# Kernel optimization log

Hardware: AMD Instinct MI355X
Metric: run time of the kernel (lower is better)

The kernel has to match this reference:

```python
import jax, jax.numpy as jnp
import numpy as np

T, B, D, H, O = 512, 256, 1024, 1024, 5


def setup_inputs() -> dict:
    key = jax.random.key(0)
    ks = jax.random.split(key, 7)
    s = 1.0 / np.sqrt(H).astype(np.float32)
    u = lambda k, shape: jax.random.uniform(k, shape, jnp.float32, -s, s)
    return {
        "input": jax.random.normal(ks[0], (T, B, D), jnp.float32),
        "hidden": jnp.zeros((B, H), jnp.float32),
        "state": jnp.zeros((B, H), jnp.float32),
        "W_in": u(ks[1], (H, D)),   # input_scale (Linear(hidden,hidden); D==H)
        "b_in": u(ks[2], (H,)),
        "W_h": u(ks[3], (H, H)),    # hidden_scale
        "b_h": u(ks[4], (H,)),
        "W_o": u(ks[5], (O, H)),    # h2o
        "b_o": u(ks[6], (O,)),
    }


def reference(input, hidden, state, W_in, b_in, W_h, b_h, W_o, b_o):
    # Dropout(0.5) is identity in eval mode.
    # Per timestep: h = sigmoid(hidden_scale(h) + input_scale(x_t))
    def step(h, x_t):
        e = x_t @ W_in.T + b_in              # [B, H]
        h = jax.nn.sigmoid(h @ W_h.T + b_h + e)
        return h, None

    hidden, _ = jax.lax.scan(step, hidden, input)  # scan over T
    out = jax.nn.log_softmax(hidden @ W_o.T + b_o, axis=-1)  # [B, O]
    return (out, hidden, state)
```

## Files before the change

kernel.cpp:

```cpp
#include <hip/hip_runtime.h>

#define T_STEPS 512
#define BATCH   256
#define DIM     1024
#define NOUT    5
#define BH      (BATCH*DIM)

typedef short s16x8 __attribute__((ext_vector_type(8)));
typedef float f32x4 __attribute__((ext_vector_type(4)));
typedef unsigned short u16;
typedef unsigned int   u32;

__device__ __forceinline__ u16 f2bf(float f) {
    union { float f; u32 u; } v; v.f = f;
    u32 r = v.u + 0x7FFFu + ((v.u >> 16) & 1u);
    return (u16)(r >> 16);
}
__device__ __forceinline__ float bf2f(u16 u) {
    union { u32 u; float f; } v; v.u = ((u32)u) << 16;
    return v.f;
}
__device__ __forceinline__ s16x8 cvt8(float4 a, float4 b) {
    s16x8 v;
    v[0]=(short)f2bf(a.x); v[1]=(short)f2bf(a.y); v[2]=(short)f2bf(a.z); v[3]=(short)f2bf(a.w);
    v[4]=(short)f2bf(b.x); v[5]=(short)f2bf(b.y); v[6]=(short)f2bf(b.z); v[7]=(short)f2bf(b.w);
    return v;
}

__device__ __forceinline__ void ldg_cv16_issue(const u16* p, s16x8* dst) {
    asm volatile("global_load_dwordx4 %0, %1, off sc0 sc1"
                 : "=v"(*dst) : "v"(p) : "memory");
}
__device__ __forceinline__ void stg_cv8(u16* p, ushort4 v) {
    asm volatile("global_store_dwordx2 %0, %1, off sc0 sc1"
                 :: "v"(p), "v"(v) : "memory");
}
__device__ __forceinline__ void stg_cv4(u32* p, u32 v) {
    asm volatile("global_store_dword %0, %1, off sc0 sc1"
                 :: "v"(p), "v"(v) : "memory");
}
__device__ __forceinline__ void wait_vm0() {
    asm volatile("s_waitcnt vmcnt(0)" ::: "memory");
}

__global__ __launch_bounds__(256) void cvt_kernel(const float* __restrict__ src,
                                                  u16* __restrict__ dst, int n4) {
    int i = blockIdx.x * 256 + threadIdx.x;
    if (i < n4) {
        float4 x = ((const float4*)src)[i];
        ushort4 o;
        o.x = f2bf(x.x); o.y = f2bf(x.y); o.z = f2bf(x.z); o.w = f2bf(x.w);
        ((ushort4*)dst)[i] = o;
    }
}

#define PADA 88

__global__ __launch_bounds__(256, 2) void gemm_e(
    const float* __restrict__ X,
    const u16*   __restrict__ Wb,
    const float* __restrict__ b_in,
    u16*         __restrict__ E)
{
    __shared__ u16 sA[128 * PADA];
    __shared__ u16 sB[128 * 64];

    const int K = 1024;
    int tid  = threadIdx.x;
    int lane = tid & 63, wv = tid >> 6;
    int lm   = lane & 15, quad = lane >> 4;

    int bid = blockIdx.x;
    int xcd = bid & 7;
    int s   = bid >> 3;
    int bn  = s & 7;
    int bm  = (s >> 3) * 8 + xcd;

    int wm   = wv >> 1, wn = wv & 1;

    float bias[4];
#pragma unroll
    for (int nt = 0; nt < 4; ++nt)
        bias[nt] = b_in[bn*128 + wn*64 + nt*16 + lm];

    f32x4 acc[4][4];
#pragma unroll
    for (int a = 0; a < 4; ++a)
#pragma unroll
        for (int b = 0; b < 4; ++b)
            acc[a][b] = (f32x4){0.f, 0.f, 0.f, 0.f};

    int colB  = (lane & 7) ^ (lane >> 3);
    int rowB0 = lane >> 3;

    for (int kk = 0; kk < K; kk += 64) {
#pragma unroll
        for (int i = 0; i < 4; ++i) {
            int q   = i*4 + wv;
            int row = q*8 + rowB0;
            const u16* gp = Wb + (size_t)(bn*128 + row)*K + kk + colB*8;
            __builtin_amdgcn_global_load_lds(
                (const __attribute__((address_space(1))) void*)gp,
                (__attribute__((address_space(3))) void*)(sB + q*512),
                16, 0, 0);
        }
#pragma unroll
        for (int p = 0; p < 4; ++p) {
            int row = (tid >> 3) + 32*p;
            int k8  = (tid & 7) * 8;
            const float* gp = X + (size_t)(bm*128 + row)*K + kk + k8;
            float4 x0 = ((const float4*)gp)[0];
            float4 x1 = ((const float4*)gp)[1];
            *(s16x8*)&sA[row*PADA + k8] = cvt8(x0, x1);
        }
        __syncthreads();
#pragma unroll
        for (int kc = 0; kc < 2; ++kc) {
            s16x8 af[4], bfr[4];
#pragma unroll
            for (int mt = 0; mt < 4; ++mt) {
                int row = wm*64 + mt*16 + lm;
                af[mt] = *(const s16x8*)&sA[row*PADA + kc*32 + quad*8];
            }
            int c8 = kc*4 + quad;
#pragma unroll
            for (int nt = 0; nt < 4; ++nt) {
                int row = wn*64 + nt*16 + lm;
                bfr[nt] = *(const s16x8*)&sB[row*64 + ((c8 ^ (row & 7)) * 8)];
            }
#pragma unroll
            for (int mt = 0; mt < 4; ++mt)
#pragma unroll
                for (int nt = 0; nt < 4; ++nt)
                    acc[mt][nt] = __builtin_amdgcn_mfma_f32_16x16x32_bf16(
                        af[mt], bfr[nt], acc[mt][nt], 0, 0, 0);
        }
        __syncthreads();
    }
#pragma unroll
    for (int mt = 0; mt < 4; ++mt)
#pragma unroll
        for (int nt = 0; nt < 4; ++nt)
#pragma unroll
            for (int i = 0; i < 4; ++i) {
                int row = bm*128 + wm*64 + mt*16 + quad*4 + i;
                int col = bn*128 + wn*64 + nt*16 + lm;
                E[(size_t)row*1024 + col] = f2bf(acc[mt][nt][i] + bias[nt]);
            }
}

__global__ __launch_bounds__(256, 1) void rnn_phase2(
    const float* __restrict__ h0,
    const float* __restrict__ Wh,
    const float* __restrict__ bh,
    const u16*   __restrict__ E,
    u16*         __restrict__ hbuf,
    u32*         __restrict__ flags,
    float*       __restrict__ hidden_out)
{
    __shared__ float red[4][16][68];
    int tid  = threadIdx.x;
    int lane = tid & 63, wv = tid >> 6;
    int lm   = lane & 15, quad = lane >> 4;
    int r    = blockIdx.x >> 4, c = blockIdx.x & 15;

    s16x8 wf[4][8];
#pragma unroll
    for (int ct = 0; ct < 4; ++ct)
#pragma unroll
        for (int kc = 0; kc < 8; ++kc) {
            int n = c*64 + ct*16 + lm;
            int k = wv*256 + kc*32 + quad*8;
            const float* p = Wh + (size_t)n*1024 + k;
            float4 x0 = ((const float4*)p)[0];
            float4 x1 = ((const float4*)p)[1];
            wf[ct][kc] = cvt8(x0, x1);
        }

    int m  = tid >> 4;
    int n4 = (tid & 15) * 4;
    float4 bh4 = *(const float4*)&bh[c*64 + n4];
    int rowA = r*16 + lm;
    const u32* fpoll = flags + (size_t)(r*16 + lm)*16;
    u32*       fown  = flags + (size_t)(r*16 + c)*16;

    for (int t = 0; t < T_STEPS; ++t) {
        ushort4 e4 = *(const ushort4*)&E[(size_t)t*BH + (size_t)(r*16 + m)*1024 + c*64 + n4];

        if (t > 0) {
            u32 target = (u32)t;
            for (;;) {
                u32 v;
                asm volatile("global_load_dword %0, %1, off sc0 sc1"
                             : "=v"(v) : "v"(fpoll) : "memory");
                asm volatile("s_waitcnt vmcnt(0)" ::: "memory");
                if (__all(v >= target)) break;
                __builtin_amdgcn_s_sleep(1);
            }
        }

        s16x8 af[8];
        if (t == 0) {
#pragma unroll
            for (int kc = 0; kc < 8; ++kc) {
                const float* p = h0 + (size_t)rowA*1024 + wv*256 + kc*32 + quad*8;
                float4 x0 = ((const float4*)p)[0];
                float4 x1 = ((const float4*)p)[1];
                af[kc] = cvt8(x0, x1);
            }
        } else {
            const u16* hb = hbuf + (size_t)(t & 1)*BH;
#pragma unroll
            for (int kc = 0; kc < 8; ++kc)
                ldg_cv16_issue(&hb[(size_t)rowA*1024 + wv*256 + kc*32 + quad*8], &af[kc]);
            asm volatile("s_waitcnt vmcnt(0)"
                         : "+v"(af[0]), "+v"(af[1]), "+v"(af[2]), "+v"(af[3]),
                           "+v"(af[4]), "+v"(af[5]), "+v"(af[6]), "+v"(af[7])
                         :: "memory");
        }

        f32x4 acc[4];
#pragma unroll
        for (int ct = 0; ct < 4; ++ct) acc[ct] = (f32x4){0.f, 0.f, 0.f, 0.f};
#pragma unroll
        for (int kc = 0; kc < 8; ++kc)
#pragma unroll
            for (int ct = 0; ct < 4; ++ct)
                acc[ct] = __builtin_amdgcn_mfma_f32_16x16x32_bf16(af[kc], wf[ct][kc], acc[ct], 0, 0, 0);

#pragma unroll
        for (int ct = 0; ct < 4; ++ct)
#pragma unroll
            for (int i = 0; i < 4; ++i)
                red[wv][quad*4 + i][ct*16 + lm] = acc[ct][i];
        __syncthreads();

        float4 p0 = *(const float4*)&red[0][m][n4];
        float4 p1 = *(const float4*)&red[1][m][n4];
        float4 p2 = *(const float4*)&red[2][m][n4];
        float4 p3 = *(const float4*)&red[3][m][n4];
        float4 s;
        s.x = p0.x + p1.x + p2.x + p3.x + bh4.x + bf2f(e4.x);
        s.y = p0.y + p1.y + p2.y + p3.y + bh4.y + bf2f(e4.y);
        s.z = p0.z + p1.z + p2.z + p3.z + bh4.z + bf2f(e4.z);
        s.w = p0.w + p1.w + p2.w + p3.w + bh4.w + bf2f(e4.w);
        float4 h;
        h.x = 1.f / (1.f + __expf(-s.x));
        h.y = 1.f / (1.f + __expf(-s.y));
        h.z = 1.f / (1.f + __expf(-s.z));
        h.w = 1.f / (1.f + __expf(-s.w));

        if (t < T_STEPS - 1) {
            ushort4 hb4;
            hb4.x = f2bf(h.x); hb4.y = f2bf(h.y); hb4.z = f2bf(h.z); hb4.w = f2bf(h.w);
            stg_cv8(&hbuf[(size_t)((t + 1) & 1)*BH + (size_t)(r*16 + m)*1024 + c*64 + n4], hb4);
        } else {
            *(float4*)&hidden_out[(size_t)(r*16 + m)*1024 + c*64 + n4] = h;
        }

        wait_vm0();
        __syncthreads();
        if (tid == 0 && t < T_STEPS - 1)
            stg_cv4(fown, (u32)(t + 1));
    }
}

__global__ __launch_bounds__(64) void head_kernel(const float* __restrict__ h,
                                                  const float* __restrict__ Wo,
                                                  const float* __restrict__ bo,
                                                  float* __restrict__ out)
{
    int b = blockIdx.x, l = threadIdx.x;
    float a0 = 0.f, a1 = 0.f, a2 = 0.f, a3 = 0.f, a4 = 0.f;
    for (int k = l; k < DIM; k += 64) {
        float hv = h[b*DIM + k];
        a0 += hv * Wo[0*DIM + k];
        a1 += hv * Wo[1*DIM + k];
        a2 += hv * Wo[2*DIM + k];
        a3 += hv * Wo[3*DIM + k];
        a4 += hv * Wo[4*DIM + k];
    }
#pragma unroll
    for (int off = 32; off >= 1; off >>= 1) {
        a0 += __shfl_down(a0, off);
        a1 += __shfl_down(a1, off);
        a2 += __shfl_down(a2, off);
        a3 += __shfl_down(a3, off);
        a4 += __shfl_down(a4, off);
    }
    if (l == 0) {
        float v[5] = {a0 + bo[0], a1 + bo[1], a2 + bo[2], a3 + bo[3], a4 + bo[4]};
        float mx = v[0];
#pragma unroll
        for (int o = 1; o < 5; ++o) mx = fmaxf(mx, v[o]);
        float sum = 0.f;
#pragma unroll
        for (int o = 0; o < 5; ++o) sum += __expf(v[o] - mx);
        float lse = mx + __logf(sum);
#pragma unroll
        for (int o = 0; o < 5; ++o) out[b*NOUT + o] = v[o] - lse;
    }
}

extern "C" void kernel_launch(void* const* d_in, const int* in_sizes, int n_in,
                              void* d_out, int out_size, void* d_ws, size_t ws_size,
                              hipStream_t stream)
{
    const float* X   = (const float*)d_in[0];
    const float* h0  = (const float*)d_in[1];
    const float* st  = (const float*)d_in[2];
    const float* Win = (const float*)d_in[3];
    const float* bin = (const float*)d_in[4];
    const float* Wh  = (const float*)d_in[5];
    const float* bhp = (const float*)d_in[6];
    const float* Wo  = (const float*)d_in[7];
    const float* bo  = (const float*)d_in[8];

    char* ws    = (char*)d_ws;
    u32*  flags = (u32*)ws;
    u16*  hbuf  = (u16*)(ws + 32768);
    u16*  Wbf   = (u16*)(ws + 32768 + (size_t)2*BH*2);
    u16*  E     = (u16*)(ws + 32768 + (size_t)2*BH*2 + (size_t)DIM*DIM*2);

    float* out_lp = (float*)d_out;
    float* out_h  = out_lp + BATCH*NOUT;
    float* out_st = out_h + BH;

    hipMemsetAsync(flags, 0, 32768, stream);
    cvt_kernel<<<(DIM*DIM/4 + 255)/256, 256, 0, stream>>>(Win, Wbf, DIM*DIM/4);
    gemm_e<<<(T_STEPS*BATCH/128)*8, 256, 0, stream>>>(X, Wbf, bin, E);
    rnn_phase2<<<256, 256, 0, stream>>>(h0, Wh, bhp, E, hbuf, flags, out_h);
    head_kernel<<<BATCH, 64, 0, stream>>>(out_h, Wo, bo, out_lp);
    hipMemcpyAsync(out_st, st, (size_t)BH*sizeof(float), hipMemcpyDeviceToDevice, stream);
}
```

Baseline: 2.730 ms.

## Pre-convert X to bf16 for the E GEMM; use per-wave flags in the recurrence

Adds a separate pass that converts the input sequence to bf16 and a new GEMM that loads both operands straight into LDS with global_load_lds, used when the workspace is large enough. In the recurrent kernel, the partial-sum LDS buffer is double-buffered by timestep parity and the trailing block barrier is removed. Each wave now publishes its own completion flag after its stores drain, and pollers check those per-wave flags. The E load is also moved to after the poll. These changes aim to cut per-step barrier latency in the serial loop and speed up the input projection, at the cost of an extra full pass over X and more workspace.

```diff
diff --git a/kernel.cpp b/kernel.cpp
--- a/kernel.cpp
+++ b/kernel.cpp
@@ -5,6 +5,7 @@
 #define DIM     1024
 #define NOUT    5
 #define BH      (BATCH*DIM)
+#define TB      (T_STEPS*BATCH)
 
 typedef short s16x8 __attribute__((ext_vector_type(8)));
 typedef float f32x4 __attribute__((ext_vector_type(4)));
@@ -54,6 +55,105 @@
     }
 }
 
+__global__ __launch_bounds__(256) void cvt_x(const float* __restrict__ src,
+                                             u16* __restrict__ dst, int n8) {
+    int i = blockIdx.x * 256 + threadIdx.x;
+    if (i < n8) {
+        float4 a = ((const float4*)src)[2*i];
+        float4 b = ((const float4*)src)[2*i + 1];
+        *(s16x8*)&dst[(size_t)i*8] = cvt8(a, b);
+    }
+}
+
+__global__ __launch_bounds__(256, 2) void gemm_e_bf(
+    const u16*   __restrict__ Xb,
+    const u16*   __restrict__ Wb,
+    const float* __restrict__ b_in,
+    u16*         __restrict__ E)
+{
+    __shared__ u16 sA[128 * 64];
+    __shared__ u16 sB[128 * 64];
+
+    const int K = 1024;
+    int tid  = threadIdx.x;
+    int lane = tid & 63, wv = tid >> 6;
+    int lm   = lane & 15, quad = lane >> 4;
+
+    int bid = blockIdx.x;
+    int xcd = bid & 7;
+    int s   = bid >> 3;
+    int bn  = s & 7;
+    int bm  = (s >> 3) * 8 + xcd;
+
+    int wm = wv >> 1, wn = wv & 1;
+
+    float bias[4];
+#pragma unroll
+    for (int nt = 0; nt < 4; ++nt)
+        bias[nt] = b_in[bn*128 + wn*64 + nt*16 + lm];
+
+    f32x4 acc[4][4];
+#pragma unroll
+    for (int a = 0; a < 4; ++a)
+#pragma unroll
+        for (int b = 0; b < 4; ++b)
+            acc[a][b] = (f32x4){0.f, 0.f, 0.f, 0.f};
+
+    int colX  = (lane & 7) ^ (lane >> 3);
+    int rowX0 = lane >> 3;
+
+    for (int kk = 0; kk < K; kk += 64) {
+#pragma unroll
+        for (int i = 0; i < 4; ++i) {
+            int q   = i*4 + wv;
+            int row = q*8 + rowX0;
+            const u16* gpB = Wb + (size_t)(bn*128 + row)*K + kk + colX*8;
+            __builtin_amdgcn_global_load_lds(
+                (const __attribute__((address_space(1))) void*)gpB,
+                (__attribute__((address_space(3))) void*)(sB + q*512),
+                16, 0, 0);
+            const u16* gpA = Xb + (size_t)(bm*128 + row)*K + kk + colX*8;
+            __builtin_amdgcn_global_load_lds(
+                (const __attribute__((address_space(1))) void*)gpA,
+                (__attribute__((address_space(3))) void*)(sA + q*512),
+                16, 0, 0);
+        }
+        __syncthreads();
+#pragma unroll
+        for (int kc = 0; kc < 2; ++kc) {
+            s16x8 af[4], bfr[4];
+            int c8 = kc*4 + quad;
+#pragma unroll
+            for (int mt = 0; mt < 4; ++mt) {
+                int row = wm*64 + mt*16 + lm;
+                af[mt] = *(const s16x8*)&sA[row*64 + ((c8 ^ (row & 7)) * 8)];
+            }
+#pragma unroll
+            for (int nt = 0; nt < 4; ++nt) {
+                int row = wn*64 + nt*16 + lm;
+                bfr[nt] = *(const s16x8*)&sB[row*64 + ((c8 ^ (row & 7)) * 8)];
+            }
+#pragma unroll
+            for (int mt = 0; mt < 4; ++mt)
+#pragma unroll
+                for (int nt = 0; nt < 4; ++nt)
+                    acc[mt][nt] = __builtin_amdgcn_mfma_f32_16x16x32_bf16(
+                        af[mt], bfr[nt], acc[mt][nt], 0, 0, 0);
+        }
+        __syncthreads();
+    }
+#pragma unroll
+    for (int mt = 0; mt < 4; ++mt)
+#pragma unroll
+        for (int nt = 0; nt < 4; ++nt)
+#pragma unroll
+            for (int i = 0; i < 4; ++i) {
+                int row = bm*128 + wm*64 + mt*16 + quad*4 + i;
+                int col = bn*128 + wn*64 + nt*16 + lm;
+                E[(size_t)row*1024 + col] = f2bf(acc[mt][nt][i] + bias[nt]);
+            }
+}
+
 #define PADA 88
 
 __global__ __launch_bounds__(256, 2) void gemm_e(
@@ -76,7 +176,7 @@
     int bn  = s & 7;
     int bm  = (s >> 3) * 8 + xcd;
 
-    int wm   = wv >> 1, wn = wv & 1;
+    int wm = wv >> 1, wn = wv & 1;
 
     float bias[4];
 #pragma unroll
@@ -158,7 +258,7 @@
     u32*         __restrict__ flags,
     float*       __restrict__ hidden_out)
 {
-    __shared__ float red[4][16][68];
+    __shared__ float red[2][4][16][68];
     int tid  = threadIdx.x;
     int lane = tid & 63, wv = tid >> 6;
     int lm   = lane & 15, quad = lane >> 4;
@@ -181,12 +281,10 @@
     int n4 = (tid & 15) * 4;
     float4 bh4 = *(const float4*)&bh[c*64 + n4];
     int rowA = r*16 + lm;
-    const u32* fpoll = flags + (size_t)(r*16 + lm)*16;
-    u32*       fown  = flags + (size_t)(r*16 + c)*16;
+    const u32* fpoll = flags + (size_t)(r*16 + wv*4 + (lane & 3))*16 + ((lane >> 2) & 3)*4;
+    u32* fown = flags + (size_t)(r*16 + c)*16 + wv*4;
 
     for (int t = 0; t < T_STEPS; ++t) {
-        ushort4 e4 = *(const ushort4*)&E[(size_t)t*BH + (size_t)(r*16 + m)*1024 + c*64 + n4];
-
         if (t > 0) {
             u32 target = (u32)t;
             for (;;) {
@@ -199,6 +297,8 @@
             }
         }
 
+        ushort4 e4 = *(const ushort4*)&E[(size_t)t*BH + (size_t)(r*16 + m)*1024 + c*64 + n4];
+
         s16x8 af[8];
         if (t == 0) {
 #pragma unroll
@@ -232,13 +332,13 @@
         for (int ct = 0; ct < 4; ++ct)
 #pragma unroll
             for (int i = 0; i < 4; ++i)
-                red[wv][quad*4 + i][ct*16 + lm] = acc[ct][i];
+                red[t & 1][wv][quad*4 + i][ct*16 + lm] = acc[ct][i];
         __syncthreads();
 
-        float4 p0 = *(const float4*)&red[0][m][n4];
-        float4 p1 = *(const float4*)&red[1][m][n4];
-        float4 p2 = *(const float4*)&red[2][m][n4];
-        float4 p3 = *(const float4*)&red[3][m][n4];
+        float4 p0 = *(const float4*)&red[t & 1][0][m][n4];
+        float4 p1 = *(const float4*)&red[t & 1][1][m][n4];
+        float4 p2 = *(const float4*)&red[t & 1][2][m][n4];
+        float4 p3 = *(const float4*)&red[t & 1][3][m][n4];
         float4 s;
         s.x = p0.x + p1.x + p2.x + p3.x + bh4.x + bf2f(e4.x);
         s.y = p0.y + p1.y + p2.y + p3.y + bh4.y + bf2f(e4.y);
@@ -259,8 +359,7 @@
         }
 
         wait_vm0();
-        __syncthreads();
-        if (tid == 0 && t < T_STEPS - 1)
+        if (lane == 0 && t < T_STEPS - 1)
             stg_cv4(fown, (u32)(t + 1));
     }
 }
@@ -316,11 +415,18 @@
     const float* Wo  = (const float*)d_in[7];
     const float* bo  = (const float*)d_in[8];
 
-    char* ws    = (char*)d_ws;
-    u32*  flags = (u32*)ws;
-    u16*  hbuf  = (u16*)(ws + 32768);
-    u16*  Wbf   = (u16*)(ws + 32768 + (size_t)2*BH*2);
-    u16*  E     = (u16*)(ws + 32768 + (size_t)2*BH*2 + (size_t)DIM*DIM*2);
+    char*  ws      = (char*)d_ws;
+    size_t off_hb  = 32768;
+    size_t off_wb  = off_hb + (size_t)2*BH*2;
+    size_t off_e   = off_wb + (size_t)DIM*DIM*2;
+    size_t off_xb  = off_e + (size_t)TB*DIM*2;
+    size_t need_bf = off_xb + (size_t)TB*DIM*2;
+
+    u32* flags = (u32*)ws;
+    u16* hbuf  = (u16*)(ws + off_hb);
+    u16* Wbf   = (u16*)(ws + off_wb);
+    u16* E     = (u16*)(ws + off_e);
+    u16* Xbf   = (u16*)(ws + off_xb);
 
     float* out_lp = (float*)d_out;
     float* out_h  = out_lp + BATCH*NOUT;
@@ -328,7 +434,14 @@
 
     hipMemsetAsync(flags, 0, 32768, stream);
     cvt_kernel<<<(DIM*DIM/4 + 255)/256, 256, 0, stream>>>(Win, Wbf, DIM*DIM/4);
-    gemm_e<<<(T_STEPS*BATCH/128)*8, 256, 0, stream>>>(X, Wbf, bin, E);
+
+    if (ws_size >= need_bf) {
+        cvt_x<<<(TB*DIM/8)/256, 256, 0, stream>>>(X, Xbf, TB*DIM/8);
+        gemm_e_bf<<<(TB/128)*8, 256, 0, stream>>>(Xbf, Wbf, bin, E);
+    } else {
+        gemm_e<<<(TB/128)*8, 256, 0, stream>>>(X, Wbf, bin, E);
+    }
+
     rnn_phase2<<<256, 256, 0, stream>>>(h0, Wh, bhp, E, hbuf, flags, out_h);
     head_kernel<<<BATCH, 64, 0, stream>>>(out_h, Wo, bo, out_lp);
     hipMemcpyAsync(out_st, st, (size_t)BH*sizeof(float), hipMemcpyDeviceToDevice, stream);
```

New measurement: 2.857 ms. +4.7%, slower.
